# Kernel optimization log

Measured on AMD Instinct MI355X. Metric: run time of the kernel, lower is better.

## Reference

```python
import jax, jax.numpy as jnp
import numpy as np

N_NODES = 100000
N_EDGES = 1600000
EMBED_DIM = 128
HIDDEN_DIM = 256


def setup_inputs() -> dict:
    key = jax.random.key(0)
    k_emb, k_src, k_dst, k_w1, k_w2 = jax.random.split(key, 5)
    emb = jax.random.normal(k_emb, (N_NODES, EMBED_DIM), dtype=jnp.float32)
    edge_src = jax.random.randint(k_src, (N_EDGES,), 0, N_NODES)
    edge_dst = jax.random.randint(k_dst, (N_EDGES,), 0, N_NODES)
    # Linear(2D -> H) and Linear(H -> D), stored as [in, out] for x @ W
    W1 = jax.random.normal(k_w1, (2 * EMBED_DIM, HIDDEN_DIM), dtype=jnp.float32) * (1.0 / np.sqrt(2 * EMBED_DIM))
    b1 = jnp.zeros((HIDDEN_DIM,), dtype=jnp.float32)
    W2 = jax.random.normal(k_w2, (HIDDEN_DIM, EMBED_DIM), dtype=jnp.float32) * (1.0 / np.sqrt(HIDDEN_DIM))
    b2 = jnp.zeros((EMBED_DIM,), dtype=jnp.float32)
    return {"emb": emb, "edge_src": edge_src, "edge_dst": edge_dst,
            "W1": W1, "b1": b1, "W2": W2, "b2": b2}


def reference(emb, edge_src, edge_dst, W1, b1, W2, b2):
    N, D = emb.shape
    E = edge_src.shape[0]
    # gather neighbor embeddings and segment-mean per destination node
    gathered = emb[edge_src]                                    # [E, D]
    nbr_sum = jax.ops.segment_sum(gathered, edge_dst, num_segments=N)   # [N, D]
    counts = jax.ops.segment_sum(jnp.ones((E,), emb.dtype), edge_dst, num_segments=N)  # [N]
    nbr_mean = nbr_sum / jnp.maximum(counts, 1.0)[:, None]
    # nodes with no neighbors fall back to their own embedding
    nbr_mean = jnp.where(counts[:, None] == 0, emb, nbr_mean)
    concat = jnp.concatenate([emb, nbr_mean], axis=-1)          # [N, 2D]
    h = jax.nn.relu(concat @ W1 + b1)                           # [N, H]
    return h @ W2 + b2                                          # [N, D]
```

## Files before the change

kernel.cpp:

```cpp
#include <hip/hip_runtime.h>

#define DD 128
#define HH 256
#define K1 256
#define BM 64
#define CH 2048
#define CH1 4096
#define CAP 8192

typedef __bf16 bf16;
typedef __attribute__((ext_vector_type(8))) __bf16 bf16x8;
typedef __attribute__((ext_vector_type(4))) float f32x4;
typedef __attribute__((ext_vector_type(2))) float f32x2;


__global__ __launch_bounds__(256) void count512_k(const int* __restrict__ dst,
                                                  int* __restrict__ bcnt,
                                                  int E, int BSH) {
    __shared__ int c[512];
    for (int j = threadIdx.x; j < 512; j += 256) c[j] = 0;
    __syncthreads();
    for (int e = blockIdx.x * 256 + threadIdx.x; e < E; e += gridDim.x * 256)
        atomicAdd(&c[dst[e] >> BSH], 1);
    __syncthreads();
    for (int j = threadIdx.x; j < 512; j += 256)
        if (c[j]) atomicAdd(&bcnt[j], c[j]);
}

__global__ __launch_bounds__(512) void scan512_k(const int* __restrict__ bcnt,
                                                 int* __restrict__ bbase,
                                                 int* __restrict__ bpos,
                                                 int NB, int E) {
    __shared__ int s[512];
    const int t = threadIdx.x;
    int v = (t < NB) ? bcnt[t] : 0;
    s[t] = v;
    __syncthreads();
    for (int off = 1; off < 512; off <<= 1) {
        int y = (t >= off) ? s[t - off] : 0;
        __syncthreads();
        s[t] += y;
        __syncthreads();
    }
    int excl = s[t] - v;
    if (t < NB) { bbase[t] = excl; bpos[t] = excl; }
    if (t == 0) bbase[NB] = E;
}

__global__ __launch_bounds__(256) void part512_k(const int* __restrict__ src,
                                                 const int* __restrict__ dst,
                                                 int* __restrict__ bpos,
                                                 int2* __restrict__ pairs,
                                                 int E, int BSH) {
    __shared__ int lcnt[512];
    __shared__ int lbase[512];
    const int t = threadIdx.x;
    const int e0 = blockIdx.x * CH1;
    const int e1 = min(E, e0 + CH1);
    for (int j = t; j < 512; j += 256) lcnt[j] = 0;
    __syncthreads();
    int rs[CH1 / 256];
    #pragma unroll
    for (int k = 0; k < CH1 / 256; ++k) {
        int e = e0 + k * 256 + t;
        int b = -1;
        if (e < e1) { b = dst[e] >> BSH; atomicAdd(&lcnt[b], 1); }
        rs[k] = b;
    }
    __syncthreads();
    for (int j = t; j < 512; j += 256) {
        int c = lcnt[j];
        lbase[j] = c ? atomicAdd(&bpos[j], c) : 0;
        lcnt[j] = 0;
    }
    __syncthreads();
    #pragma unroll
    for (int k = 0; k < CH1 / 256; ++k) {
        int e = e0 + k * 256 + t;
        if (e < e1) {
            int b = rs[k];
            int slot = lbase[b] + atomicAdd(&lcnt[b], 1);
            pairs[slot] = make_int2(src[e], dst[e]);
        }
    }
}

__global__ __launch_bounds__(256) void sortb_k(const int2* __restrict__ pairs,
                                               const int* __restrict__ bbase,
                                               int* __restrict__ offs,
                                               int* __restrict__ ssrc,
                                               int N, int BSH) {
    __shared__ int hist[512];
    __shared__ int pref[512];
    __shared__ int run[512];
    __shared__ int sorted[CAP];
    const int t = threadIdx.x;
    const int b = blockIdx.x;
    const int B = 1 << BSH;
    const int d0 = b << BSH;
    const int nd = min(B, N - d0);
    const int rb = bbase[b], re = bbase[b + 1];
    const int cntE = re - rb;
    for (int j = t; j < 512; j += 256) hist[j] = 0;
    __syncthreads();
    for (int i = rb + t; i < re; i += 256)
        atomicAdd(&hist[pairs[i].y - d0], 1);
    __syncthreads();
    for (int j = t; j < 512; j += 256) pref[j] = hist[j];
    __syncthreads();
    for (int off = 1; off < 512; off <<= 1) {
        int j2 = t + 256;
        int v0 = (t >= off) ? pref[t - off] : 0;
        int v1 = (j2 >= off) ? pref[j2 - off] : 0;
        __syncthreads();
        pref[t] += v0;
        pref[j2] += v1;
        __syncthreads();
    }
    for (int j = t; j < nd; j += 256) offs[d0 + j] = rb + pref[j];
    for (int j = t; j < 512; j += 256) run[j] = pref[j] - hist[j];
    __syncthreads();
    if (cntE <= CAP) {
        for (int i = rb + t; i < re; i += 256) {
            int2 p = pairs[i];
            int pos = atomicAdd(&run[p.y - d0], 1);
            sorted[pos] = p.x;
        }
        __syncthreads();
        for (int i = t; i < cntE; i += 256) ssrc[rb + i] = sorted[i];
    } else {
        for (int i = rb + t; i < re; i += 256) {
            int2 p = pairs[i];
            int pos = atomicAdd(&run[p.y - d0], 1);
            ssrc[rb + pos] = p.x;
        }
    }
}


__global__ __launch_bounds__(256) void hist_k(const int* __restrict__ dst,
                                              int* __restrict__ cnt, int E) {
    for (int e = blockIdx.x * blockDim.x + threadIdx.x; e < E;
         e += gridDim.x * blockDim.x)
        atomicAdd(&cnt[dst[e]], 1);
}

__global__ __launch_bounds__(256) void scan1_k(const int* __restrict__ cnt,
                                               int* __restrict__ offs,
                                               int* __restrict__ part, int N) {
    __shared__ int sdata[256];
    const int b = blockIdx.x, t = threadIdx.x;
    const int base = b * 1024 + t * 4;
    int v[4], sum = 0;
    #pragma unroll
    for (int i = 0; i < 4; ++i) {
        int idx = base + i;
        v[i] = (idx < N) ? cnt[idx] : 0;
        sum += v[i];
    }
    sdata[t] = sum;
    __syncthreads();
    for (int off = 1; off < 256; off <<= 1) {
        int y = (t >= off) ? sdata[t - off] : 0;
        __syncthreads();
        sdata[t] += y;
        __syncthreads();
    }
    int excl = sdata[t] - sum;
    if (t == 255) part[b] = sdata[255];
    int run = excl;
    #pragma unroll
    for (int i = 0; i < 4; ++i) {
        int idx = base + i;
        if (idx < N) offs[idx] = run;
        run += v[i];
    }
}

__global__ __launch_bounds__(128) void scan2_k(int* __restrict__ part, int nparts) {
    __shared__ int sdata[128];
    const int t = threadIdx.x;
    int v = (t < nparts) ? part[t] : 0;
    sdata[t] = v;
    __syncthreads();
    for (int off = 1; off < 128; off <<= 1) {
        int y = (t >= off) ? sdata[t - off] : 0;
        __syncthreads();
        sdata[t] += y;
        __syncthreads();
    }
    if (t < nparts) part[t] = sdata[t] - v;
}

__global__ __launch_bounds__(256) void scan3_k(int* __restrict__ offs,
                                               const int* __restrict__ part, int N) {
    for (int i = blockIdx.x * blockDim.x + threadIdx.x; i < N;
         i += gridDim.x * blockDim.x)
        offs[i] += part[i >> 10];
}

__global__ __launch_bounds__(256) void bucket_k(const int* __restrict__ src,
                                                const int* __restrict__ dst,
                                                int* __restrict__ offs,
                                                int* __restrict__ ssrc,
                                                int E, int N) {
    const int r = blockIdx.x & 7;
    const int chunk = blockIdx.x >> 3;
    const int lo = r * (N >> 3);
    const int hi = (r == 7) ? N : lo + (N >> 3);
    const int e0 = chunk * CH;
    const int e1 = min(E, e0 + CH);
    for (int e = e0 + threadIdx.x; e < e1; e += 256) {
        int d = dst[e];
        if (d >= lo && d < hi) {
            int pos = atomicAdd(&offs[d], 1);
            ssrc[pos] = src[e];
        }
    }
}

__global__ __launch_bounds__(256) void cvt8_k(const float* __restrict__ emb,
                                              unsigned* __restrict__ emb8,
                                              size_t n8) {
    for (size_t i = blockIdx.x * blockDim.x + threadIdx.x; i < n8;
         i += (size_t)gridDim.x * blockDim.x) {
        float4 a = *reinterpret_cast<const float4*>(&emb[i * 8]);
        float4 b = *reinterpret_cast<const float4*>(&emb[i * 8 + 4]);
        int w0 = __builtin_amdgcn_cvt_pk_fp8_f32(a.x, a.y, 0, false);
        w0 = __builtin_amdgcn_cvt_pk_fp8_f32(a.z, a.w, w0, true);
        int w1 = __builtin_amdgcn_cvt_pk_fp8_f32(b.x, b.y, 0, false);
        w1 = __builtin_amdgcn_cvt_pk_fp8_f32(b.z, b.w, w1, true);
        uint2 o; o.x = (unsigned)w0; o.y = (unsigned)w1;
        *reinterpret_cast<uint2*>(&emb8[i * 2]) = o;
    }
}

__global__ __launch_bounds__(256) void gather8_k(const unsigned* __restrict__ emb8,
                                                 const float* __restrict__ emb,
                                                 const int* __restrict__ offs,
                                                 const int* __restrict__ ssrc,
                                                 bf16* __restrict__ nbrh, int N) {
    const int wid = threadIdx.x >> 6;
    const int lane = threadIdx.x & 63;
    const int d = blockIdx.x * 4 + wid;
    if (d >= N) return;
    const int slot = lane >> 4;
    const int c8 = (lane & 15) * 8;
    const int start = (d == 0) ? 0 : offs[d - 1];
    const int end = offs[d];
    float acc[8];
    #pragma unroll
    for (int j = 0; j < 8; ++j) acc[j] = 0.f;
    int e = start;
    for (; e + 8 <= end; e += 8) {
        int s0 = ssrc[e + slot];
        int s1 = ssrc[e + 4 + slot];
        uint2 v0 = *reinterpret_cast<const uint2*>(&emb8[((size_t)s0 * DD + c8) >> 2]);
        uint2 v1 = *reinterpret_cast<const uint2*>(&emb8[((size_t)s1 * DD + c8) >> 2]);
        f32x2 p;
        p = __builtin_amdgcn_cvt_pk_f32_fp8(v0.x, false); acc[0] += p[0]; acc[1] += p[1];
        p = __builtin_amdgcn_cvt_pk_f32_fp8(v0.x, true);  acc[2] += p[0]; acc[3] += p[1];
        p = __builtin_amdgcn_cvt_pk_f32_fp8(v0.y, false); acc[4] += p[0]; acc[5] += p[1];
        p = __builtin_amdgcn_cvt_pk_f32_fp8(v0.y, true);  acc[6] += p[0]; acc[7] += p[1];
        p = __builtin_amdgcn_cvt_pk_f32_fp8(v1.x, false); acc[0] += p[0]; acc[1] += p[1];
        p = __builtin_amdgcn_cvt_pk_f32_fp8(v1.x, true);  acc[2] += p[0]; acc[3] += p[1];
        p = __builtin_amdgcn_cvt_pk_f32_fp8(v1.y, false); acc[4] += p[0]; acc[5] += p[1];
        p = __builtin_amdgcn_cvt_pk_f32_fp8(v1.y, true);  acc[6] += p[0]; acc[7] += p[1];
    }
    for (; e + 4 <= end; e += 4) {
        int s0 = ssrc[e + slot];
        uint2 v0 = *reinterpret_cast<const uint2*>(&emb8[((size_t)s0 * DD + c8) >> 2]);
        f32x2 p;
        p = __builtin_amdgcn_cvt_pk_f32_fp8(v0.x, false); acc[0] += p[0]; acc[1] += p[1];
        p = __builtin_amdgcn_cvt_pk_f32_fp8(v0.x, true);  acc[2] += p[0]; acc[3] += p[1];
        p = __builtin_amdgcn_cvt_pk_f32_fp8(v0.y, false); acc[4] += p[0]; acc[5] += p[1];
        p = __builtin_amdgcn_cvt_pk_f32_fp8(v0.y, true);  acc[6] += p[0]; acc[7] += p[1];
    }
    if (slot < end - e) {
        int s0 = ssrc[e + slot];
        uint2 v0 = *reinterpret_cast<const uint2*>(&emb8[((size_t)s0 * DD + c8) >> 2]);
        f32x2 p;
        p = __builtin_amdgcn_cvt_pk_f32_fp8(v0.x, false); acc[0] += p[0]; acc[1] += p[1];
        p = __builtin_amdgcn_cvt_pk_f32_fp8(v0.x, true);  acc[2] += p[0]; acc[3] += p[1];
        p = __builtin_amdgcn_cvt_pk_f32_fp8(v0.y, false); acc[4] += p[0]; acc[5] += p[1];
        p = __builtin_amdgcn_cvt_pk_f32_fp8(v0.y, true);  acc[6] += p[0]; acc[7] += p[1];
    }
    #pragma unroll
    for (int j = 0; j < 8; ++j) {
        acc[j] += __shfl_xor(acc[j], 16);
        acc[j] += __shfl_xor(acc[j], 32);
    }
    if (slot == 0) {
        bf16x8 o;
        if (end > start) {
            float inv = 1.f / (float)(end - start);
            #pragma unroll
            for (int j = 0; j < 8; ++j) o[j] = (bf16)(acc[j] * inv);
        } else {
            float4 a = *reinterpret_cast<const float4*>(&emb[(size_t)d * DD + c8]);
            float4 b = *reinterpret_cast<const float4*>(&emb[(size_t)d * DD + c8 + 4]);
            o[0]=(bf16)a.x; o[1]=(bf16)a.y; o[2]=(bf16)a.z; o[3]=(bf16)a.w;
            o[4]=(bf16)b.x; o[5]=(bf16)b.y; o[6]=(bf16)b.z; o[7]=(bf16)b.w;
        }
        *reinterpret_cast<bf16x8*>(&nbrh[(size_t)d * DD + c8]) = o;
    }
}

__global__ __launch_bounds__(256) void gather_k(const float* __restrict__ emb,
                                                const int* __restrict__ offs,
                                                const int* __restrict__ ssrc,
                                                float* __restrict__ nbr, int N) {
    const int wid = threadIdx.x >> 6;
    const int lane = threadIdx.x & 63;
    const int d = blockIdx.x * 4 + wid;
    if (d >= N) return;
    const int sub = lane >> 5;
    const int c = (lane & 31) * 4;
    const int start = (d == 0) ? 0 : offs[d - 1];
    const int end = offs[d];
    float4 acc = make_float4(0.f, 0.f, 0.f, 0.f);
    int e = start;
    for (; e + 4 <= end; e += 4) {
        int s0 = ssrc[e + sub];
        int s1 = ssrc[e + 2 + sub];
        float4 v0 = *reinterpret_cast<const float4*>(&emb[(size_t)s0 * DD + c]);
        float4 v1 = *reinterpret_cast<const float4*>(&emb[(size_t)s1 * DD + c]);
        acc.x += v0.x + v1.x; acc.y += v0.y + v1.y;
        acc.z += v0.z + v1.z; acc.w += v0.w + v1.w;
    }
    for (; e + 2 <= end; e += 2) {
        int s = ssrc[e + sub];
        float4 v = *reinterpret_cast<const float4*>(&emb[(size_t)s * DD + c]);
        acc.x += v.x; acc.y += v.y; acc.z += v.z; acc.w += v.w;
    }
    if (e < end && sub == 0) {
        int s = ssrc[e];
        float4 v = *reinterpret_cast<const float4*>(&emb[(size_t)s * DD + c]);
        acc.x += v.x; acc.y += v.y; acc.z += v.z; acc.w += v.w;
    }
    acc.x += __shfl_xor(acc.x, 32);
    acc.y += __shfl_xor(acc.y, 32);
    acc.z += __shfl_xor(acc.z, 32);
    acc.w += __shfl_xor(acc.w, 32);
    if (sub == 0) {
        if (end > start) {
            float inv = 1.f / (float)(end - start);
            acc.x *= inv; acc.y *= inv; acc.z *= inv; acc.w *= inv;
        } else {
            acc = *reinterpret_cast<const float4*>(&emb[(size_t)d * DD + c]);
        }
        *reinterpret_cast<float4*>(&nbr[(size_t)d * DD + c]) = acc;
    }
}

__global__ __launch_bounds__(64) void pack_k(const float* __restrict__ W, int NC,
                                             bf16* __restrict__ hi) {
    const int ntiles = NC >> 4;
    const int kt = blockIdx.x / ntiles;
    const int nt = blockIdx.x % ntiles;
    const int l = threadIdx.x;
    const int k0 = kt * 32 + (l >> 4) * 8;
    const int n = nt * 16 + (l & 15);
    bf16x8 hv;
    #pragma unroll
    for (int r = 0; r < 8; ++r)
        hv[r] = (bf16)W[(size_t)(k0 + r) * NC + n];
    *reinterpret_cast<bf16x8*>(hi + ((size_t)blockIdx.x * 64 + l) * 8) = hv;
}

__global__ __launch_bounds__(256) void mlp_mfma_k(const float* __restrict__ emb,
        const float* nbrf, const bf16* __restrict__ nbrh,
        const bf16* __restrict__ w1h, const float* __restrict__ b1,
        const bf16* __restrict__ w2h, const float* __restrict__ b2,
        float* out, int N) {
    __shared__ char smem[BM * K1 * 2];
    const int t = threadIdx.x;
    const int n0 = blockIdx.x * BM;
    const int l = t & 63;
    const int w = t >> 6;

    #pragma unroll
    for (int i = 0; i < 8; ++i) {
        int chunk = i * 256 + t;
        int row = chunk >> 5;
        int c0 = (chunk & 31) * 8;
        int n = n0 + row;
        bf16x8 hv;
        if (n < N) {
            if (c0 >= DD && nbrh != nullptr) {
                hv = *reinterpret_cast<const bf16x8*>(&nbrh[(size_t)n * DD + (c0 - DD)]);
            } else {
                const float* sp = (c0 < DD) ? &emb[(size_t)n * DD + c0]
                                            : &nbrf[(size_t)n * DD + (c0 - DD)];
                float4 a = *reinterpret_cast<const float4*>(sp);
                float4 b = *reinterpret_cast<const float4*>(sp + 4);
                hv[0]=(bf16)a.x; hv[1]=(bf16)a.y; hv[2]=(bf16)a.z; hv[3]=(bf16)a.w;
                hv[4]=(bf16)b.x; hv[5]=(bf16)b.y; hv[6]=(bf16)b.z; hv[7]=(bf16)b.w;
            }
        } else {
            #pragma unroll
            for (int j = 0; j < 8; ++j) hv[j] = (bf16)0.f;
        }
        int off = row * 512 + ((c0 * 2) ^ ((row & 7) << 4));
        *reinterpret_cast<bf16x8*>(smem + off) = hv;
    }
    __syncthreads();

    const int arow = l & 15;
    const int abyte = (l >> 4) * 16;

    f32x4 acc[4][4];
    #pragma unroll
    for (int ntl = 0; ntl < 4; ++ntl) {
        float bv = b1[w * 64 + ntl * 16 + (l & 15)];
        #pragma unroll
        for (int mt = 0; mt < 4; ++mt)
            acc[mt][ntl] = (f32x4){bv, bv, bv, bv};
    }
    for (int kt = 0; kt < 8; ++kt) {
        bf16x8 ah[4];
        #pragma unroll
        for (int mt = 0; mt < 4; ++mt) {
            int row = mt * 16 + arow;
            int off = row * 512 + ((kt * 64 + abyte) ^ ((row & 7) << 4));
            ah[mt] = *reinterpret_cast<const bf16x8*>(smem + off);
        }
        #pragma unroll
        for (int ntl = 0; ntl < 4; ++ntl) {
            int nt = w * 4 + ntl;
            size_t boff = ((size_t)(kt * 16 + nt) * 64 + l) * 8;
            bf16x8 bh = *reinterpret_cast<const bf16x8*>(w1h + boff);
            #pragma unroll
            for (int mt = 0; mt < 4; ++mt)
                acc[mt][ntl] = __builtin_amdgcn_mfma_f32_16x16x32_bf16(ah[mt], bh, acc[mt][ntl], 0, 0, 0);
        }
    }
    __syncthreads();

    #pragma unroll
    for (int mt = 0; mt < 4; ++mt)
        #pragma unroll
        for (int ntl = 0; ntl < 4; ++ntl) {
            int col = w * 64 + ntl * 16 + (l & 15);
            #pragma unroll
            for (int r = 0; r < 4; ++r) {
                int row = mt * 16 + (l >> 4) * 4 + r;
                int off = row * 512 + ((col * 2) ^ ((row & 7) << 4));
                *reinterpret_cast<bf16*>(smem + off) = (bf16)fmaxf(acc[mt][ntl][r], 0.f);
            }
        }
    __syncthreads();

    f32x4 acc2[4][2];
    #pragma unroll
    for (int ntl = 0; ntl < 2; ++ntl) {
        float bv = b2[w * 32 + ntl * 16 + (l & 15)];
        #pragma unroll
        for (int mt = 0; mt < 4; ++mt)
            acc2[mt][ntl] = (f32x4){bv, bv, bv, bv};
    }
    for (int kt = 0; kt < 8; ++kt) {
        bf16x8 ah[4];
        #pragma unroll
        for (int mt = 0; mt < 4; ++mt) {
            int row = mt * 16 + arow;
            int off = row * 512 + ((kt * 64 + abyte) ^ ((row & 7) << 4));
            ah[mt] = *reinterpret_cast<const bf16x8*>(smem + off);
        }
        #pragma unroll
        for (int ntl = 0; ntl < 2; ++ntl) {
            int nt = w * 2 + ntl;
            size_t boff = ((size_t)(kt * 8 + nt) * 64 + l) * 8;
            bf16x8 bh = *reinterpret_cast<const bf16x8*>(w2h + boff);
            #pragma unroll
            for (int mt = 0; mt < 4; ++mt)
                acc2[mt][ntl] = __builtin_amdgcn_mfma_f32_16x16x32_bf16(ah[mt], bh, acc2[mt][ntl], 0, 0, 0);
        }
    }
    #pragma unroll
    for (int mt = 0; mt < 4; ++mt)
        #pragma unroll
        for (int ntl = 0; ntl < 2; ++ntl) {
            int col = w * 32 + ntl * 16 + (l & 15);
            #pragma unroll
            for (int r = 0; r < 4; ++r) {
                int row = mt * 16 + (l >> 4) * 4 + r;
                int n = n0 + row;
                if (n < N) out[(size_t)n * DD + col] = acc2[mt][ntl][r];
            }
        }
}

__global__ __launch_bounds__(256) void scatter_k(const float* __restrict__ emb,
        const int* __restrict__ src, const int* __restrict__ dst,
        float* nbr, float* __restrict__ cnt, int E) {
    int e = blockIdx.x * 8 + (threadIdx.x >> 5);
    if (e >= E) return;
    int lane = threadIdx.x & 31;
    int s = src[e];
    int d = dst[e];
    const float4 v = *reinterpret_cast<const float4*>(&emb[(size_t)s * DD + lane * 4]);
    float* o = &nbr[(size_t)d * DD + lane * 4];
    atomicAdd(o + 0, v.x);
    atomicAdd(o + 1, v.y);
    atomicAdd(o + 2, v.z);
    atomicAdd(o + 3, v.w);
    if (lane == 0) atomicAdd(&cnt[d], 1.0f);
}

__global__ __launch_bounds__(256) void mlp_k(const float* __restrict__ emb,
        const float* nbr, const float* cnt,
        const float* __restrict__ W1, const float* __restrict__ b1,
        const float* __restrict__ W2, const float* __restrict__ b2,
        float* out, int N) {
    __shared__ float smem[BM * K1];
    const int t = threadIdx.x;
    const int n0 = blockIdx.x * BM;
    #pragma unroll
    for (int it = 0; it < 16; ++it) {
        int idx = it * 256 + t;
        int r = idx >> 6;
        int c4 = idx & 63;
        int n = n0 + r;
        float4 v = make_float4(0.f, 0.f, 0.f, 0.f);
        if (n < N) {
            if (c4 < 32) {
                v = *reinterpret_cast<const float4*>(&emb[(size_t)n * DD + c4 * 4]);
            } else {
                float c = cnt[n];
                if (c > 0.f) {
                    v = *reinterpret_cast<const float4*>(&nbr[(size_t)n * DD + (c4 - 32) * 4]);
                    float inv = 1.f / c;
                    v.x *= inv; v.y *= inv; v.z *= inv; v.w *= inv;
                } else {
                    v = *reinterpret_cast<const float4*>(&emb[(size_t)n * DD + (c4 - 32) * 4]);
                }
            }
        }
        *reinterpret_cast<float4*>(&smem[idx * 4]) = v;
    }
    __syncthreads();
    const int tx = t & 31;
    const int ty = t >> 5;
    const int r0 = ty * 8;
    {
        const int c0 = tx * 8;
        float acc[8][8];
        const float4 bva = *reinterpret_cast<const float4*>(&b1[c0]);
        const float4 bvb = *reinterpret_cast<const float4*>(&b1[c0 + 4]);
        #pragma unroll
        for (int i = 0; i < 8; ++i) {
            acc[i][0] = bva.x; acc[i][1] = bva.y; acc[i][2] = bva.z; acc[i][3] = bva.w;
            acc[i][4] = bvb.x; acc[i][5] = bvb.y; acc[i][6] = bvb.z; acc[i][7] = bvb.w;
        }
        for (int k0 = 0; k0 < K1; k0 += 4) {
            float xs[8][4];
            #pragma unroll
            for (int i = 0; i < 8; ++i) {
                float4 xv = *reinterpret_cast<const float4*>(&smem[(r0 + i) * K1 + k0]);
                xs[i][0] = xv.x; xs[i][1] = xv.y; xs[i][2] = xv.z; xs[i][3] = xv.w;
            }
            #pragma unroll
            for (int kk = 0; kk < 4; ++kk) {
                const float4 wa = *reinterpret_cast<const float4*>(&W1[(size_t)(k0 + kk) * HH + c0]);
                const float4 wb = *reinterpret_cast<const float4*>(&W1[(size_t)(k0 + kk) * HH + c0 + 4]);
                #pragma unroll
                for (int i = 0; i < 8; ++i) {
                    float x = xs[i][kk];
                    acc[i][0] += x * wa.x; acc[i][1] += x * wa.y;
                    acc[i][2] += x * wa.z; acc[i][3] += x * wa.w;
                    acc[i][4] += x * wb.x; acc[i][5] += x * wb.y;
                    acc[i][6] += x * wb.z; acc[i][7] += x * wb.w;
                }
            }
        }
        __syncthreads();
        #pragma unroll
        for (int i = 0; i < 8; ++i) {
            float4 h0, h1;
            h0.x = fmaxf(acc[i][0], 0.f); h0.y = fmaxf(acc[i][1], 0.f);
            h0.z = fmaxf(acc[i][2], 0.f); h0.w = fmaxf(acc[i][3], 0.f);
            h1.x = fmaxf(acc[i][4], 0.f); h1.y = fmaxf(acc[i][5], 0.f);
            h1.z = fmaxf(acc[i][6], 0.f); h1.w = fmaxf(acc[i][7], 0.f);
            *reinterpret_cast<float4*>(&smem[(r0 + i) * HH + c0]) = h0;
            *reinterpret_cast<float4*>(&smem[(r0 + i) * HH + c0 + 4]) = h1;
        }
        __syncthreads();
    }
    {
        const int c0 = tx * 4;
        float acc[8][4];
        const float4 bv = *reinterpret_cast<const float4*>(&b2[c0]);
        #pragma unroll
        for (int i = 0; i < 8; ++i) {
            acc[i][0] = bv.x; acc[i][1] = bv.y; acc[i][2] = bv.z; acc[i][3] = bv.w;
        }
        for (int k0 = 0; k0 < HH; k0 += 4) {
            float hs[8][4];
            #pragma unroll
            for (int i = 0; i < 8; ++i) {
                float4 hv = *reinterpret_cast<const float4*>(&smem[(r0 + i) * HH + k0]);
                hs[i][0] = hv.x; hs[i][1] = hv.y; hs[i][2] = hv.z; hs[i][3] = hv.w;
            }
            #pragma unroll
            for (int kk = 0; kk < 4; ++kk) {
                const float4 w2 = *reinterpret_cast<const float4*>(&W2[(size_t)(k0 + kk) * DD + c0]);
                #pragma unroll
                for (int i = 0; i < 8; ++i) {
                    float h = hs[i][kk];
                    acc[i][0] += h * w2.x; acc[i][1] += h * w2.y;
                    acc[i][2] += h * w2.z; acc[i][3] += h * w2.w;
                }
            }
        }
        #pragma unroll
        for (int i = 0; i < 8; ++i) {
            int n = n0 + r0 + i;
            if (n < N) {
                float4 o;
                o.x = acc[i][0]; o.y = acc[i][1]; o.z = acc[i][2]; o.w = acc[i][3];
                *reinterpret_cast<float4*>(&out[(size_t)n * DD + c0]) = o;
            }
        }
    }
}

extern "C" void kernel_launch(void* const* d_in, const int* in_sizes, int n_in,
                              void* d_out, int out_size, void* d_ws, size_t ws_size,
                              hipStream_t stream) {
    const float* emb = (const float*)d_in[0];
    const int* esrc  = (const int*)d_in[1];
    const int* edst  = (const int*)d_in[2];
    const float* W1  = (const float*)d_in[3];
    const float* b1  = (const float*)d_in[4];
    const float* W2  = (const float*)d_in[5];
    const float* b2  = (const float*)d_in[6];
    float* out = (float*)d_out;

    const int N = in_sizes[0] / DD;
    const int E = in_sizes[1];
    const int nparts = (N + 1023) / 1024;

    int BSH = 0;
    while ((((size_t)N + ((size_t)1 << BSH) - 1) >> BSH) > 512) ++BSH;
    const int B = 1 << BSH;
    const int NB = (N + B - 1) >> BSH;

    int* cnt  = (int*)d_ws;
    int* offs = cnt + N;
    int* part = offs + N;
    int* aux  = part + 128;
    int* ssrc = aux + 2048;
    char* wp = (char*)(ssrc + E);
    wp = (char*)(((uintptr_t)wp + 15) & ~(uintptr_t)15);
    bf16* w1h = (bf16*)wp;
    bf16* w2h = w1h + 65536;
    unsigned* emb8 = (unsigned*)(w2h + 32768);
    bf16* nbrh = (bf16*)(emb8 + (size_t)N * DD / 4);
    int2* pairs = (int2*)nbrh;
    int* bcnt  = aux;
    int* bbase = aux + 512;
    int* bpos  = aux + 1280;
    const size_t need_base = (size_t)((char*)(w2h + 32768) - (char*)d_ws);
    const size_t need_full = (size_t)((char*)(nbrh + (size_t)N * DD) - (char*)d_ws);
    const bool pairs_fit = ((size_t)E * sizeof(int2) <= (size_t)N * DD * sizeof(bf16));

    if (ws_size >= need_base && nparts <= 128) {
        const bool fast = (ws_size >= need_full) && pairs_fit && (B <= 512) && ((N & 7) == 0);
        pack_k<<<dim3(128), dim3(64), 0, stream>>>(W1, HH, w1h);
        pack_k<<<dim3(64), dim3(64), 0, stream>>>(W2, DD, w2h);
        if (fast) {
            hipMemsetAsync(bcnt, 0, 512 * sizeof(int), stream);
            count512_k<<<dim3(512), dim3(256), 0, stream>>>(edst, bcnt, E, BSH);
            scan512_k<<<dim3(1), dim3(512), 0, stream>>>(bcnt, bbase, bpos, NB, E);
            part512_k<<<dim3((E + CH1 - 1) / CH1), dim3(256), 0, stream>>>(
                esrc, edst, bpos, pairs, E, BSH);
            sortb_k<<<dim3(NB), dim3(256), 0, stream>>>(pairs, bbase, offs, ssrc, N, BSH);
            cvt8_k<<<dim3(2048), dim3(256), 0, stream>>>(emb, emb8, (size_t)N * DD / 8);
            gather8_k<<<dim3((N + 3) / 4), dim3(256), 0, stream>>>(emb8, emb, offs, ssrc, nbrh, N);
            mlp_mfma_k<<<dim3((N + BM - 1) / BM), dim3(256), 0, stream>>>(
                emb, nullptr, nbrh, w1h, b1, w2h, b2, out, N);
        } else {
            hipMemsetAsync(cnt, 0, (size_t)N * sizeof(int), stream);
            hist_k<<<dim3(1024), dim3(256), 0, stream>>>(edst, cnt, E);
            scan1_k<<<dim3(nparts), dim3(256), 0, stream>>>(cnt, offs, part, N);
            scan2_k<<<dim3(1), dim3(128), 0, stream>>>(part, nparts);
            scan3_k<<<dim3(512), dim3(256), 0, stream>>>(offs, part, N);
            const int nchunks = (E + CH - 1) / CH;
            bucket_k<<<dim3(nchunks * 8), dim3(256), 0, stream>>>(esrc, edst, offs, ssrc, E, N);
            gather_k<<<dim3((N + 3) / 4), dim3(256), 0, stream>>>(emb, offs, ssrc, out, N);
            mlp_mfma_k<<<dim3((N + BM - 1) / BM), dim3(256), 0, stream>>>(
                emb, out, nullptr, w1h, b1, w2h, b2, out, N);
        }
    } else {
        float* fcnt = (float*)d_ws;
        hipMemsetAsync(out, 0, (size_t)N * DD * sizeof(float), stream);
        hipMemsetAsync(fcnt, 0, (size_t)N * sizeof(float), stream);
        scatter_k<<<dim3((E + 7) / 8), dim3(256), 0, stream>>>(emb, esrc, edst, out, fcnt, E);
        mlp_k<<<dim3((N + BM - 1) / BM), dim3(256), 0, stream>>>(
            emb, out, fcnt, W1, b1, W2, b2, out, N);
    }
}
```

Baseline: 173.0 us.

## Pack edge pairs into 32-bit keys, use finer buckets, widen MLP blocks

The partition pass now stores each edge as one 32-bit word, with the destination offset inside its bucket in the top 8 bits and the source in the low 24 bits. This halves the pairs traffic, and the pairs now live in the emb8 region. Bucket count rises to 1024 with 256 nodes per bucket, so sortb_k works on smaller per-block histograms and a smaller shared sort buffer. The two weight-pack launches are merged into one, and the MLP kernel now uses 512 threads so each wave owns fewer output columns. The new path adds limits on N (below 2^24) and on bucket size, and halving CAP may push more buckets onto the global-scatter fallback.

Result: no change. 169.8 us (-1.9%).

```diff
diff --git a/kernel.cpp b/kernel.cpp
--- a/kernel.cpp
+++ b/kernel.cpp
@@ -5,8 +5,8 @@
 #define K1 256
 #define BM 64
 #define CH 2048
-#define CH1 4096
-#define CAP 8192
+#define CH1 2048
+#define CAP 4096
 
 typedef __bf16 bf16;
 typedef __attribute__((ext_vector_type(8))) __bf16 bf16x8;
@@ -14,29 +14,29 @@
 typedef __attribute__((ext_vector_type(2))) float f32x2;
 
 
-__global__ __launch_bounds__(256) void count512_k(const int* __restrict__ dst,
-                                                  int* __restrict__ bcnt,
-                                                  int E, int BSH) {
-    __shared__ int c[512];
-    for (int j = threadIdx.x; j < 512; j += 256) c[j] = 0;
+__global__ __launch_bounds__(256) void countb_k(const int* __restrict__ dst,
+                                                int* __restrict__ bcnt,
+                                                int E, int BSH) {
+    __shared__ int c[1024];
+    for (int j = threadIdx.x; j < 1024; j += 256) c[j] = 0;
     __syncthreads();
     for (int e = blockIdx.x * 256 + threadIdx.x; e < E; e += gridDim.x * 256)
         atomicAdd(&c[dst[e] >> BSH], 1);
     __syncthreads();
-    for (int j = threadIdx.x; j < 512; j += 256)
+    for (int j = threadIdx.x; j < 1024; j += 256)
         if (c[j]) atomicAdd(&bcnt[j], c[j]);
 }
 
-__global__ __launch_bounds__(512) void scan512_k(const int* __restrict__ bcnt,
-                                                 int* __restrict__ bbase,
-                                                 int* __restrict__ bpos,
-                                                 int NB, int E) {
-    __shared__ int s[512];
+__global__ __launch_bounds__(1024) void scanb_k(const int* __restrict__ bcnt,
+                                                int* __restrict__ bbase,
+                                                int* __restrict__ bpos,
+                                                int NB, int E) {
+    __shared__ int s[1024];
     const int t = threadIdx.x;
     int v = (t < NB) ? bcnt[t] : 0;
     s[t] = v;
     __syncthreads();
-    for (int off = 1; off < 512; off <<= 1) {
+    for (int off = 1; off < 1024; off <<= 1) {
         int y = (t >= off) ? s[t - off] : 0;
         __syncthreads();
         s[t] += y;
@@ -47,17 +47,17 @@
     if (t == 0) bbase[NB] = E;
 }
 
-__global__ __launch_bounds__(256) void part512_k(const int* __restrict__ src,
-                                                 const int* __restrict__ dst,
-                                                 int* __restrict__ bpos,
-                                                 int2* __restrict__ pairs,
-                                                 int E, int BSH) {
-    __shared__ int lcnt[512];
-    __shared__ int lbase[512];
+__global__ __launch_bounds__(256) void part_k(const int* __restrict__ src,
+                                              const int* __restrict__ dst,
+                                              int* __restrict__ bpos,
+                                              unsigned* __restrict__ pairs,
+                                              int E, int BSH, int Bm1) {
+    __shared__ int lcnt[1024];
+    __shared__ int lbase[1024];
     const int t = threadIdx.x;
     const int e0 = blockIdx.x * CH1;
     const int e1 = min(E, e0 + CH1);
-    for (int j = t; j < 512; j += 256) lcnt[j] = 0;
+    for (int j = t; j < 1024; j += 256) lcnt[j] = 0;
     __syncthreads();
     int rs[CH1 / 256];
     #pragma unroll
@@ -68,7 +68,7 @@
         rs[k] = b;
     }
     __syncthreads();
-    for (int j = t; j < 512; j += 256) {
+    for (int j = t; j < 1024; j += 256) {
         int c = lcnt[j];
         lbase[j] = c ? atomicAdd(&bpos[j], c) : 0;
         lcnt[j] = 0;
@@ -80,19 +80,19 @@
         if (e < e1) {
             int b = rs[k];
             int slot = lbase[b] + atomicAdd(&lcnt[b], 1);
-            pairs[slot] = make_int2(src[e], dst[e]);
-        }
-    }
-}
-
-__global__ __launch_bounds__(256) void sortb_k(const int2* __restrict__ pairs,
+            pairs[slot] = ((unsigned)(dst[e] & Bm1) << 24) | (unsigned)src[e];
+        }
+    }
+}
+
+__global__ __launch_bounds__(256) void sortb_k(const unsigned* __restrict__ pairs,
                                                const int* __restrict__ bbase,
                                                int* __restrict__ offs,
                                                int* __restrict__ ssrc,
                                                int N, int BSH) {
-    __shared__ int hist[512];
-    __shared__ int pref[512];
-    __shared__ int run[512];
+    __shared__ int hist[256];
+    __shared__ int pref[256];
+    __shared__ int run[256];
     __shared__ int sorted[CAP];
     const int t = threadIdx.x;
     const int b = blockIdx.x;
@@ -101,38 +101,35 @@
     const int nd = min(B, N - d0);
     const int rb = bbase[b], re = bbase[b + 1];
     const int cntE = re - rb;
-    for (int j = t; j < 512; j += 256) hist[j] = 0;
+    hist[t] = 0;
     __syncthreads();
     for (int i = rb + t; i < re; i += 256)
-        atomicAdd(&hist[pairs[i].y - d0], 1);
-    __syncthreads();
-    for (int j = t; j < 512; j += 256) pref[j] = hist[j];
-    __syncthreads();
-    for (int off = 1; off < 512; off <<= 1) {
-        int j2 = t + 256;
-        int v0 = (t >= off) ? pref[t - off] : 0;
-        int v1 = (j2 >= off) ? pref[j2 - off] : 0;
-        __syncthreads();
-        pref[t] += v0;
-        pref[j2] += v1;
-        __syncthreads();
-    }
-    for (int j = t; j < nd; j += 256) offs[d0 + j] = rb + pref[j];
-    for (int j = t; j < 512; j += 256) run[j] = pref[j] - hist[j];
+        atomicAdd(&hist[pairs[i] >> 24], 1);
+    __syncthreads();
+    pref[t] = hist[t];
+    __syncthreads();
+    for (int off = 1; off < 256; off <<= 1) {
+        int y = (t >= off) ? pref[t - off] : 0;
+        __syncthreads();
+        pref[t] += y;
+        __syncthreads();
+    }
+    if (t < nd) offs[d0 + t] = rb + pref[t];
+    run[t] = pref[t] - hist[t];
     __syncthreads();
     if (cntE <= CAP) {
         for (int i = rb + t; i < re; i += 256) {
-            int2 p = pairs[i];
-            int pos = atomicAdd(&run[p.y - d0], 1);
-            sorted[pos] = p.x;
+            unsigned p = pairs[i];
+            int pos = atomicAdd(&run[p >> 24], 1);
+            sorted[pos] = (int)(p & 0xFFFFFFu);
         }
         __syncthreads();
         for (int i = t; i < cntE; i += 256) ssrc[rb + i] = sorted[i];
     } else {
         for (int i = rb + t; i < re; i += 256) {
-            int2 p = pairs[i];
-            int pos = atomicAdd(&run[p.y - d0], 1);
-            ssrc[rb + pos] = p.x;
+            unsigned p = pairs[i];
+            int pos = atomicAdd(&run[p >> 24], 1);
+            ssrc[rb + pos] = (int)(p & 0xFFFFFFu);
         }
     }
 }
@@ -216,93 +213,6 @@
             int pos = atomicAdd(&offs[d], 1);
             ssrc[pos] = src[e];
         }
-    }
-}
-
-__global__ __launch_bounds__(256) void cvt8_k(const float* __restrict__ emb,
-                                              unsigned* __restrict__ emb8,
-                                              size_t n8) {
-    for (size_t i = blockIdx.x * blockDim.x + threadIdx.x; i < n8;
-         i += (size_t)gridDim.x * blockDim.x) {
-        float4 a = *reinterpret_cast<const float4*>(&emb[i * 8]);
-        float4 b = *reinterpret_cast<const float4*>(&emb[i * 8 + 4]);
-        int w0 = __builtin_amdgcn_cvt_pk_fp8_f32(a.x, a.y, 0, false);
-        w0 = __builtin_amdgcn_cvt_pk_fp8_f32(a.z, a.w, w0, true);
-        int w1 = __builtin_amdgcn_cvt_pk_fp8_f32(b.x, b.y, 0, false);
-        w1 = __builtin_amdgcn_cvt_pk_fp8_f32(b.z, b.w, w1, true);
-        uint2 o; o.x = (unsigned)w0; o.y = (unsigned)w1;
-        *reinterpret_cast<uint2*>(&emb8[i * 2]) = o;
-    }
-}
-
-__global__ __launch_bounds__(256) void gather8_k(const unsigned* __restrict__ emb8,
-                                                 const float* __restrict__ emb,
-                                                 const int* __restrict__ offs,
-                                                 const int* __restrict__ ssrc,
-                                                 bf16* __restrict__ nbrh, int N) {
-    const int wid = threadIdx.x >> 6;
-    const int lane = threadIdx.x & 63;
-    const int d = blockIdx.x * 4 + wid;
-    if (d >= N) return;
-    const int slot = lane >> 4;
-    const int c8 = (lane & 15) * 8;
-    const int start = (d == 0) ? 0 : offs[d - 1];
-    const int end = offs[d];
-    float acc[8];
-    #pragma unroll
-    for (int j = 0; j < 8; ++j) acc[j] = 0.f;
-    int e = start;
-    for (; e + 8 <= end; e += 8) {
-        int s0 = ssrc[e + slot];
-        int s1 = ssrc[e + 4 + slot];
-        uint2 v0 = *reinterpret_cast<const uint2*>(&emb8[((size_t)s0 * DD + c8) >> 2]);
-        uint2 v1 = *reinterpret_cast<const uint2*>(&emb8[((size_t)s1 * DD + c8) >> 2]);
-        f32x2 p;
-        p = __builtin_amdgcn_cvt_pk_f32_fp8(v0.x, false); acc[0] += p[0]; acc[1] += p[1];
-        p = __builtin_amdgcn_cvt_pk_f32_fp8(v0.x, true);  acc[2] += p[0]; acc[3] += p[1];
-        p = __builtin_amdgcn_cvt_pk_f32_fp8(v0.y, false); acc[4] += p[0]; acc[5] += p[1];
-        p = __builtin_amdgcn_cvt_pk_f32_fp8(v0.y, true);  acc[6] += p[0]; acc[7] += p[1];
-        p = __builtin_amdgcn_cvt_pk_f32_fp8(v1.x, false); acc[0] += p[0]; acc[1] += p[1];
-        p = __builtin_amdgcn_cvt_pk_f32_fp8(v1.x, true);  acc[2] += p[0]; acc[3] += p[1];
-        p = __builtin_amdgcn_cvt_pk_f32_fp8(v1.y, false); acc[4] += p[0]; acc[5] += p[1];
-        p = __builtin_amdgcn_cvt_pk_f32_fp8(v1.y, true);  acc[6] += p[0]; acc[7] += p[1];
-    }
-    for (; e + 4 <= end; e += 4) {
-        int s0 = ssrc[e + slot];
-        uint2 v0 = *reinterpret_cast<const uint2*>(&emb8[((size_t)s0 * DD + c8) >> 2]);
-        f32x2 p;
-        p = __builtin_amdgcn_cvt_pk_f32_fp8(v0.x, false); acc[0] += p[0]; acc[1] += p[1];
-        p = __builtin_amdgcn_cvt_pk_f32_fp8(v0.x, true);  acc[2] += p[0]; acc[3] += p[1];
-        p = __builtin_amdgcn_cvt_pk_f32_fp8(v0.y, false); acc[4] += p[0]; acc[5] += p[1];
-        p = __builtin_amdgcn_cvt_pk_f32_fp8(v0.y, true);  acc[6] += p[0]; acc[7] += p[1];
-    }
-    if (slot < end - e) {
-        int s0 = ssrc[e + slot];
-        uint2 v0 = *reinterpret_cast<const uint2*>(&emb8[((size_t)s0 * DD + c8) >> 2]);
-        f32x2 p;
-        p = __builtin_amdgcn_cvt_pk_f32_fp8(v0.x, false); acc[0] += p[0]; acc[1] += p[1];
-        p = __builtin_amdgcn_cvt_pk_f32_fp8(v0.x, true);  acc[2] += p[0]; acc[3] += p[1];
-        p = __builtin_amdgcn_cvt_pk_f32_fp8(v0.y, false); acc[4] += p[0]; acc[5] += p[1];
-        p = __builtin_amdgcn_cvt_pk_f32_fp8(v0.y, true);  acc[6] += p[0]; acc[7] += p[1];
-    }
-    #pragma unroll
-    for (int j = 0; j < 8; ++j) {
-        acc[j] += __shfl_xor(acc[j], 16);
-        acc[j] += __shfl_xor(acc[j], 32);
-    }
-    if (slot == 0) {
-        bf16x8 o;
-        if (end > start) {
-            float inv = 1.f / (float)(end - start);
-            #pragma unroll
-            for (int j = 0; j < 8; ++j) o[j] = (bf16)(acc[j] * inv);
-        } else {
-            float4 a = *reinterpret_cast<const float4*>(&emb[(size_t)d * DD + c8]);
-            float4 b = *reinterpret_cast<const float4*>(&emb[(size_t)d * DD + c8 + 4]);
-            o[0]=(bf16)a.x; o[1]=(bf16)a.y; o[2]=(bf16)a.z; o[3]=(bf16)a.w;
-            o[4]=(bf16)b.x; o[5]=(bf16)b.y; o[6]=(bf16)b.z; o[7]=(bf16)b.w;
-        }
-        *reinterpret_cast<bf16x8*>(&nbrh[(size_t)d * DD + c8]) = o;
     }
 }
 
@@ -353,11 +263,104 @@
     }
 }
 
-__global__ __launch_bounds__(64) void pack_k(const float* __restrict__ W, int NC,
-                                             bf16* __restrict__ hi) {
+__global__ __launch_bounds__(256) void cvt8_k(const float* __restrict__ emb,
+                                              unsigned* __restrict__ emb8,
+                                              size_t n8) {
+    for (size_t i = blockIdx.x * blockDim.x + threadIdx.x; i < n8;
+         i += (size_t)gridDim.x * blockDim.x) {
+        float4 a = *reinterpret_cast<const float4*>(&emb[i * 8]);
+        float4 b = *reinterpret_cast<const float4*>(&emb[i * 8 + 4]);
+        int w0 = __builtin_amdgcn_cvt_pk_fp8_f32(a.x, a.y, 0, false);
+        w0 = __builtin_amdgcn_cvt_pk_fp8_f32(a.z, a.w, w0, true);
+        int w1 = __builtin_amdgcn_cvt_pk_fp8_f32(b.x, b.y, 0, false);
+        w1 = __builtin_amdgcn_cvt_pk_fp8_f32(b.z, b.w, w1, true);
+        uint2 o; o.x = (unsigned)w0; o.y = (unsigned)w1;
+        *reinterpret_cast<uint2*>(&emb8[i * 2]) = o;
+    }
+}
+
+__global__ __launch_bounds__(256) void gather8_k(const unsigned* __restrict__ emb8,
+                                                 const float* __restrict__ emb,
+                                                 const int* __restrict__ offs,
+                                                 const int* __restrict__ ssrc,
+                                                 bf16* __restrict__ nbrh, int N) {
+    const int wid = threadIdx.x >> 6;
+    const int lane = threadIdx.x & 63;
+    const int d = blockIdx.x * 4 + wid;
+    if (d >= N) return;
+    const int slot = lane >> 4;
+    const int c8 = (lane & 15) * 8;
+    const int start = (d == 0) ? 0 : offs[d - 1];
+    const int end = offs[d];
+    float acc[8];
+    #pragma unroll
+    for (int j = 0; j < 8; ++j) acc[j] = 0.f;
+    int e = start;
+    for (; e + 8 <= end; e += 8) {
+        int s0 = ssrc[e + slot];
+        int s1 = ssrc[e + 4 + slot];
+        uint2 v0 = *reinterpret_cast<const uint2*>(&emb8[((size_t)s0 * DD + c8) >> 2]);
+        uint2 v1 = *reinterpret_cast<const uint2*>(&emb8[((size_t)s1 * DD + c8) >> 2]);
+        f32x2 p;
+        p = __builtin_amdgcn_cvt_pk_f32_fp8(v0.x, false); acc[0] += p[0]; acc[1] += p[1];
+        p = __builtin_amdgcn_cvt_pk_f32_fp8(v0.x, true);  acc[2] += p[0]; acc[3] += p[1];
+        p = __builtin_amdgcn_cvt_pk_f32_fp8(v0.y, false); acc[4] += p[0]; acc[5] += p[1];
+        p = __builtin_amdgcn_cvt_pk_f32_fp8(v0.y, true);  acc[6] += p[0]; acc[7] += p[1];
+        p = __builtin_amdgcn_cvt_pk_f32_fp8(v1.x, false); acc[0] += p[0]; acc[1] += p[1];
+        p = __builtin_amdgcn_cvt_pk_f32_fp8(v1.x, true);  acc[2] += p[0]; acc[3] += p[1];
+        p = __builtin_amdgcn_cvt_pk_f32_fp8(v1.y, false); acc[4] += p[0]; acc[5] += p[1];
+        p = __builtin_amdgcn_cvt_pk_f32_fp8(v1.y, true);  acc[6] += p[0]; acc[7] += p[1];
+    }
+    for (; e + 4 <= end; e += 4) {
+        int s0 = ssrc[e + slot];
+        uint2 v0 = *reinterpret_cast<const uint2*>(&emb8[((size_t)s0 * DD + c8) >> 2]);
+        f32x2 p;
+        p = __builtin_amdgcn_cvt_pk_f32_fp8(v0.x, false); acc[0] += p[0]; acc[1] += p[1];
+        p = __builtin_amdgcn_cvt_pk_f32_fp8(v0.x, true);  acc[2] += p[0]; acc[3] += p[1];
+        p = __builtin_amdgcn_cvt_pk_f32_fp8(v0.y, false); acc[4] += p[0]; acc[5] += p[1];
+        p = __builtin_amdgcn_cvt_pk_f32_fp8(v0.y, true);  acc[6] += p[0]; acc[7] += p[1];
+    }
+    if (slot < end - e) {
+        int s0 = ssrc[e + slot];
+        uint2 v0 = *reinterpret_cast<const uint2*>(&emb8[((size_t)s0 * DD + c8) >> 2]);
+        f32x2 p;
+        p = __builtin_amdgcn_cvt_pk_f32_fp8(v0.x, false); acc[0] += p[0]; acc[1] += p[1];
+        p = __builtin_amdgcn_cvt_pk_f32_fp8(v0.x, true);  acc[2] += p[0]; acc[3] += p[1];
+        p = __builtin_amdgcn_cvt_pk_f32_fp8(v0.y, false); acc[4] += p[0]; acc[5] += p[1];
+        p = __builtin_amdgcn_cvt_pk_f32_fp8(v0.y, true);  acc[6] += p[0]; acc[7] += p[1];
+    }
+    #pragma unroll
+    for (int j = 0; j < 8; ++j) {
+        acc[j] += __shfl_xor(acc[j], 16);
+        acc[j] += __shfl_xor(acc[j], 32);
+    }
+    if (slot == 0) {
+        bf16x8 o;
+        if (end > start) {
+            float inv = 1.f / (float)(end - start);
+            #pragma unroll
+            for (int j = 0; j < 8; ++j) o[j] = (bf16)(acc[j] * inv);
+        } else {
+            float4 a = *reinterpret_cast<const float4*>(&emb[(size_t)d * DD + c8]);
+            float4 b = *reinterpret_cast<const float4*>(&emb[(size_t)d * DD + c8 + 4]);
+            o[0]=(bf16)a.x; o[1]=(bf16)a.y; o[2]=(bf16)a.z; o[3]=(bf16)a.w;
+            o[4]=(bf16)b.x; o[5]=(bf16)b.y; o[6]=(bf16)b.z; o[7]=(bf16)b.w;
+        }
+        *reinterpret_cast<bf16x8*>(&nbrh[(size_t)d * DD + c8]) = o;
+    }
+}
+
+__global__ __launch_bounds__(64) void packW_k(const float* __restrict__ W1,
+                                              const float* __restrict__ W2,
+                                              bf16* __restrict__ w1h,
+                                              bf16* __restrict__ w2h) {
+    const int bid = blockIdx.x;
+    const float* W; bf16* outp; int NC; int rel;
+    if (bid < 128) { W = W1; outp = w1h; NC = HH; rel = bid; }
+    else           { W = W2; outp = w2h; NC = DD; rel = bid - 128; }
     const int ntiles = NC >> 4;
-    const int kt = blockIdx.x / ntiles;
-    const int nt = blockIdx.x % ntiles;
+    const int kt = rel / ntiles;
+    const int nt = rel % ntiles;
     const int l = threadIdx.x;
     const int k0 = kt * 32 + (l >> 4) * 8;
     const int n = nt * 16 + (l & 15);
@@ -365,10 +368,10 @@
     #pragma unroll
     for (int r = 0; r < 8; ++r)
         hv[r] = (bf16)W[(size_t)(k0 + r) * NC + n];
-    *reinterpret_cast<bf16x8*>(hi + ((size_t)blockIdx.x * 64 + l) * 8) = hv;
-}
-
-__global__ __launch_bounds__(256) void mlp_mfma_k(const float* __restrict__ emb,
+    *reinterpret_cast<bf16x8*>(outp + ((size_t)rel * 64 + l) * 8) = hv;
+}
+
+__global__ __launch_bounds__(512) void mlp_mfma_k(const float* __restrict__ emb,
         const float* nbrf, const bf16* __restrict__ nbrh,
         const bf16* __restrict__ w1h, const float* __restrict__ b1,
         const bf16* __restrict__ w2h, const float* __restrict__ b2,
@@ -380,8 +383,8 @@
     const int w = t >> 6;
 
     #pragma unroll
-    for (int i = 0; i < 8; ++i) {
-        int chunk = i * 256 + t;
+    for (int i = 0; i < 4; ++i) {
+        int chunk = i * 512 + t;
         int row = chunk >> 5;
         int c0 = (chunk & 31) * 8;
         int n = n0 + row;
@@ -409,10 +412,10 @@
     const int arow = l & 15;
     const int abyte = (l >> 4) * 16;
 
-    f32x4 acc[4][4];
-    #pragma unroll
-    for (int ntl = 0; ntl < 4; ++ntl) {
-        float bv = b1[w * 64 + ntl * 16 + (l & 15)];
+    f32x4 acc[4][2];
+    #pragma unroll
+    for (int ntl = 0; ntl < 2; ++ntl) {
+        float bv = b1[w * 32 + ntl * 16 + (l & 15)];
         #pragma unroll
         for (int mt = 0; mt < 4; ++mt)
             acc[mt][ntl] = (f32x4){bv, bv, bv, bv};
@@ -426,8 +429,8 @@
             ah[mt] = *reinterpret_cast<const bf16x8*>(smem + off);
         }
         #pragma unroll
-        for (int ntl = 0; ntl < 4; ++ntl) {
-            int nt = w * 4 + ntl;
+        for (int ntl = 0; ntl < 2; ++ntl) {
+            int nt = w * 2 + ntl;
             size_t boff = ((size_t)(kt * 16 + nt) * 64 + l) * 8;
             bf16x8 bh = *reinterpret_cast<const bf16x8*>(w1h + boff);
             #pragma unroll
@@ -440,8 +443,8 @@
     #pragma unroll
     for (int mt = 0; mt < 4; ++mt)
         #pragma unroll
-        for (int ntl = 0; ntl < 4; ++ntl) {
-            int col = w * 64 + ntl * 16 + (l & 15);
+        for (int ntl = 0; ntl < 2; ++ntl) {
+            int col = w * 32 + ntl * 16 + (l & 15);
             #pragma unroll
             for (int r = 0; r < 4; ++r) {
                 int row = mt * 16 + (l >> 4) * 4 + r;
@@ -451,13 +454,12 @@
         }
     __syncthreads();
 
-    f32x4 acc2[4][2];
-    #pragma unroll
-    for (int ntl = 0; ntl < 2; ++ntl) {
-        float bv = b2[w * 32 + ntl * 16 + (l & 15)];
+    f32x4 acc2[4];
+    {
+        float bv = b2[w * 16 + (l & 15)];
         #pragma unroll
         for (int mt = 0; mt < 4; ++mt)
-            acc2[mt][ntl] = (f32x4){bv, bv, bv, bv};
+            acc2[mt] = (f32x4){bv, bv, bv, bv};
     }
     for (int kt = 0; kt < 8; ++kt) {
         bf16x8 ah[4];
@@ -467,28 +469,22 @@
             int off = row * 512 + ((kt * 64 + abyte) ^ ((row & 7) << 4));
             ah[mt] = *reinterpret_cast<const bf16x8*>(smem + off);
         }
-        #pragma unroll
-        for (int ntl = 0; ntl < 2; ++ntl) {
-            int nt = w * 2 + ntl;
-            size_t boff = ((size_t)(kt * 8 + nt) * 64 + l) * 8;
-            bf16x8 bh = *reinterpret_cast<const bf16x8*>(w2h + boff);
-            #pragma unroll
-            for (int mt = 0; mt < 4; ++mt)
-                acc2[mt][ntl] = __builtin_amdgcn_mfma_f32_16x16x32_bf16(ah[mt], bh, acc2[mt][ntl], 0, 0, 0);
-        }
-    }
-    #pragma unroll
-    for (int mt = 0; mt < 4; ++mt)
-        #pragma unroll
-        for (int ntl = 0; ntl < 2; ++ntl) {
-            int col = w * 32 + ntl * 16 + (l & 15);
-            #pragma unroll
-            for (int r = 0; r < 4; ++r) {
-                int row = mt * 16 + (l >> 4) * 4 + r;
-                int n = n0 + row;
-                if (n < N) out[(size_t)n * DD + col] = acc2[mt][ntl][r];
-            }
-        }
+        size_t boff = ((size_t)(kt * 8 + w) * 64 + l) * 8;
+        bf16x8 bh = *reinterpret_cast<const bf16x8*>(w2h + boff);
+        #pragma unroll
+        for (int mt = 0; mt < 4; ++mt)
+            acc2[mt] = __builtin_amdgcn_mfma_f32_16x16x32_bf16(ah[mt], bh, acc2[mt], 0, 0, 0);
+    }
+    #pragma unroll
+    for (int mt = 0; mt < 4; ++mt) {
+        int col = w * 16 + (l & 15);
+        #pragma unroll
+        for (int r = 0; r < 4; ++r) {
+            int row = mt * 16 + (l >> 4) * 4 + r;
+            int n = n0 + row;
+            if (n < N) out[(size_t)n * DD + col] = acc2[mt][r];
+        }
+    }
 }
 
 __global__ __launch_bounds__(256) void scatter_k(const float* __restrict__ emb,
@@ -642,7 +638,7 @@
     const int nparts = (N + 1023) / 1024;
 
     int BSH = 0;
-    while ((((size_t)N + ((size_t)1 << BSH) - 1) >> BSH) > 512) ++BSH;
+    while ((((size_t)N + ((size_t)1 << BSH) - 1) >> BSH) > 1024) ++BSH;
     const int B = 1 << BSH;
     const int NB = (N + B - 1) >> BSH;
 
@@ -650,35 +646,35 @@
     int* offs = cnt + N;
     int* part = offs + N;
     int* aux  = part + 128;
-    int* ssrc = aux + 2048;
+    int* ssrc = aux + 4096;
     char* wp = (char*)(ssrc + E);
     wp = (char*)(((uintptr_t)wp + 15) & ~(uintptr_t)15);
     bf16* w1h = (bf16*)wp;
     bf16* w2h = w1h + 65536;
     unsigned* emb8 = (unsigned*)(w2h + 32768);
     bf16* nbrh = (bf16*)(emb8 + (size_t)N * DD / 4);
-    int2* pairs = (int2*)nbrh;
+    unsigned* pairs = emb8;
     int* bcnt  = aux;
-    int* bbase = aux + 512;
-    int* bpos  = aux + 1280;
+    int* bbase = aux + 1024;
+    int* bpos  = aux + 2560;
     const size_t need_base = (size_t)((char*)(w2h + 32768) - (char*)d_ws);
     const size_t need_full = (size_t)((char*)(nbrh + (size_t)N * DD) - (char*)d_ws);
-    const bool pairs_fit = ((size_t)E * sizeof(int2) <= (size_t)N * DD * sizeof(bf16));
+    const bool pairs_fit = ((size_t)E * 4 <= (size_t)N * DD / 4 * 4 + (size_t)N * DD * 2);
 
     if (ws_size >= need_base && nparts <= 128) {
-        const bool fast = (ws_size >= need_full) && pairs_fit && (B <= 512) && ((N & 7) == 0);
-        pack_k<<<dim3(128), dim3(64), 0, stream>>>(W1, HH, w1h);
-        pack_k<<<dim3(64), dim3(64), 0, stream>>>(W2, DD, w2h);
+        const bool fast = (ws_size >= need_full) && pairs_fit && (BSH <= 8) &&
+                          (N < (1 << 24)) && ((N & 7) == 0) && (NB <= 1024);
+        packW_k<<<dim3(192), dim3(64), 0, stream>>>(W1, W2, w1h, w2h);
         if (fast) {
-            hipMemsetAsync(bcnt, 0, 512 * sizeof(int), stream);
-            count512_k<<<dim3(512), dim3(256), 0, stream>>>(edst, bcnt, E, BSH);
-            scan512_k<<<dim3(1), dim3(512), 0, stream>>>(bcnt, bbase, bpos, NB, E);
-            part512_k<<<dim3((E + CH1 - 1) / CH1), dim3(256), 0, stream>>>(
-                esrc, edst, bpos, pairs, E, BSH);
+            hipMemsetAsync(bcnt, 0, 1024 * sizeof(int), stream);
+            countb_k<<<dim3(512), dim3(256), 0, stream>>>(edst, bcnt, E, BSH);
+            scanb_k<<<dim3(1), dim3(1024), 0, stream>>>(bcnt, bbase, bpos, NB, E);
+            part_k<<<dim3((E + CH1 - 1) / CH1), dim3(256), 0, stream>>>(
+                esrc, edst, bpos, pairs, E, BSH, B - 1);
             sortb_k<<<dim3(NB), dim3(256), 0, stream>>>(pairs, bbase, offs, ssrc, N, BSH);
             cvt8_k<<<dim3(2048), dim3(256), 0, stream>>>(emb, emb8, (size_t)N * DD / 8);
             gather8_k<<<dim3((N + 3) / 4), dim3(256), 0, stream>>>(emb8, emb, offs, ssrc, nbrh, N);
-            mlp_mfma_k<<<dim3((N + BM - 1) / BM), dim3(256), 0, stream>>>(
+            mlp_mfma_k<<<dim3((N + BM - 1) / BM), dim3(512), 0, stream>>>(
                 emb, nullptr, nbrh, w1h, b1, w2h, b2, out, N);
         } else {
             hipMemsetAsync(cnt, 0, (size_t)N * sizeof(int), stream);
@@ -689,7 +685,7 @@
             const int nchunks = (E + CH - 1) / CH;
             bucket_k<<<dim3(nchunks * 8), dim3(256), 0, stream>>>(esrc, edst, offs, ssrc, E, N);
             gather_k<<<dim3((N + 3) / 4), dim3(256), 0, stream>>>(emb, offs, ssrc, out, N);
-            mlp_mfma_k<<<dim3((N + BM - 1) / BM), dim3(256), 0, stream>>>(
+            mlp_mfma_k<<<dim3((N + BM - 1) / BM), dim3(512), 0, stream>>>(
                 emb, out, nullptr, w1h, b1, w2h, b2, out, N);
         }
     } else {
```
